# Performance work log

Measured on AMD Instinct MI355X. Metric: run time of the kernel, lower is better.

## Reference

```python
import jax, jax.numpy as jnp
import numpy as np

N_NODES = 100000
N_EDGES = 1600000
IN_FEAT = 128
OUT_FEAT = 128


def setup_inputs() -> dict:
    key = jax.random.key(0)
    k1, k2, k3 = jax.random.split(key, 3)
    x = jax.random.normal(k1, (N_NODES, IN_FEAT), dtype=jnp.float32)
    W = jax.random.normal(k2, (IN_FEAT, OUT_FEAT), dtype=jnp.float32) * (1.0 / np.sqrt(IN_FEAT))
    b = jnp.zeros((OUT_FEAT,), dtype=jnp.float32)
    edge_index = jax.random.randint(k3, (2, N_EDGES), 0, N_NODES, dtype=jnp.int64)
    return {"x": x, "W": W, "b": b, "edge_index": edge_index}


def reference(x, W, b, edge_index):
    # PyG GCNConv: add self-loops, symmetric deg normalization, scatter-add.
    N = x.shape[0]
    loops = jnp.arange(N, dtype=edge_index.dtype)
    ei = jnp.concatenate([edge_index, jnp.stack([loops, loops])], axis=1)  # [2, E+N]
    row, col = ei[0], ei[1]  # source, target
    ones = jnp.ones(ei.shape[1], dtype=x.dtype)
    deg = jax.ops.segment_sum(ones, col, num_segments=N)  # in-degree incl. self-loop
    deg_inv_sqrt = jnp.where(deg > 0, jax.lax.rsqrt(deg), 0.0)
    norm = deg_inv_sqrt[row] * deg_inv_sqrt[col]  # [E+N]
    xw = x @ W  # [N, out_feat]
    msg = xw[row] * norm[:, None]  # gather + normalize
    out = jax.ops.segment_sum(msg, col, num_segments=N) + b  # scatter-add + bias
    return out
```

## Files before the change

kernel.cpp:

```cpp
#include <hip/hip_runtime.h>

#define N_NODES 100000
#define N_EDGES 1600000
#define FEAT 128
#define NBUCK 782
#define BUCK_SHIFT 7
#define BUCK_MASK 127
#define GEMM_BLOCKS 1563
#define HIST_EPB 4096
#define HIST_BLOCKS 391
#define WT_PITCH 136

typedef __attribute__((ext_vector_type(8))) short short8;
typedef __attribute__((ext_vector_type(4))) float f32x4;

__device__ inline unsigned short f2bf(float f) {
    unsigned u = __builtin_bit_cast(unsigned, f);
    unsigned r = (u + 0x7FFFu + ((u >> 16) & 1u)) >> 16;
    return (unsigned short)r;
}
__device__ inline float bf2f(unsigned h) {
    unsigned u = h << 16;
    return __builtin_bit_cast(float, u);
}

__global__ __launch_bounds__(256)
void k_gemm_hist(const float* __restrict__ x, const float* __restrict__ W,
                 unsigned short* __restrict__ yb,
                 const int* __restrict__ col, int* __restrict__ bcnt) {
    int bid = blockIdx.x, tid = threadIdx.x;
    if (bid >= GEMM_BLOCKS) {
        __shared__ int hist[NBUCK];
        for (int i = tid; i < NBUCK; i += 256) hist[i] = 0;
        __syncthreads();
        int e0 = (bid - GEMM_BLOCKS) * HIST_EPB;
        int n = min(HIST_EPB, N_EDGES - e0);
        for (int i = tid * 4; i < n; i += 1024) {
            if (i + 3 < n) {
                int4 c4 = *(const int4*)(col + e0 + i);
                atomicAdd(&hist[c4.x >> BUCK_SHIFT], 1);
                atomicAdd(&hist[c4.y >> BUCK_SHIFT], 1);
                atomicAdd(&hist[c4.z >> BUCK_SHIFT], 1);
                atomicAdd(&hist[c4.w >> BUCK_SHIFT], 1);
            } else {
                for (int j = i; j < n; ++j) atomicAdd(&hist[col[e0 + j] >> BUCK_SHIFT], 1);
            }
        }
        __syncthreads();
        for (int i = tid; i < NBUCK; i += 256) {
            int h = hist[i];
            if (h) atomicAdd(&bcnt[i], h);
        }
        return;
    }

    __shared__ unsigned short Ws[FEAT * WT_PITCH];
    for (int idx = tid; idx < FEAT * FEAT; idx += 256) {
        int k = idx >> 7, n = idx & 127;
        Ws[n * WT_PITCH + k] = f2bf(W[idx]);
    }
    __syncthreads();

    int lane = tid & 63;
    int m = lane & 15, quad = lane >> 4;
    int rowBase = bid * 64 + (tid >> 6) * 16;
    int arow = rowBase + m;
    if (arow >= N_NODES) arow = N_NODES - 1;
    const float* xr = x + (size_t)arow * FEAT + quad * 8;

    f32x4 acc[8];
#pragma unroll
    for (int nt = 0; nt < 8; ++nt) acc[nt] = (f32x4){0.f, 0.f, 0.f, 0.f};

#pragma unroll
    for (int kk = 0; kk < 4; ++kk) {
        float4 xa = *(const float4*)(xr + kk * 32);
        float4 xc = *(const float4*)(xr + kk * 32 + 4);
        short8 a;
        a[0] = (short)f2bf(xa.x); a[1] = (short)f2bf(xa.y);
        a[2] = (short)f2bf(xa.z); a[3] = (short)f2bf(xa.w);
        a[4] = (short)f2bf(xc.x); a[5] = (short)f2bf(xc.y);
        a[6] = (short)f2bf(xc.z); a[7] = (short)f2bf(xc.w);
        const unsigned short* wp = Ws + m * WT_PITCH + kk * 32 + quad * 8;
#pragma unroll
        for (int nt = 0; nt < 8; ++nt) {
            short8 bf = *(const short8*)(wp + nt * 16 * WT_PITCH);
            acc[nt] = __builtin_amdgcn_mfma_f32_16x16x32_bf16(a, bf, acc[nt], 0, 0, 0);
        }
    }

    int r0 = rowBase + quad * 4;
#pragma unroll
    for (int nt = 0; nt < 8; ++nt) {
        int cc = nt * 16 + m;
#pragma unroll
        for (int r = 0; r < 4; ++r) {
            int rr = r0 + r;
            if (rr < N_NODES) yb[(size_t)rr * FEAT + cc] = f2bf(acc[nt][r]);
        }
    }
}

__global__ __launch_bounds__(1024)
void k_bscan(const int* __restrict__ bcnt, int* __restrict__ bstarts,
             int* __restrict__ bcursor) {
    __shared__ int s[1024];
    int tid = threadIdx.x;
    int v = (tid < NBUCK) ? bcnt[tid] : 0;
    s[tid] = v;
    __syncthreads();
    for (int off = 1; off < 1024; off <<= 1) {
        int t = (tid >= off) ? s[tid - off] : 0;
        __syncthreads();
        s[tid] += t;
        __syncthreads();
    }
    if (tid < NBUCK) {
        int ex = s[tid] - v;
        bstarts[tid] = ex;
        bcursor[tid] = ex;
    }
    if (tid == NBUCK - 1) bstarts[NBUCK] = s[tid];
}

__global__ __launch_bounds__(256)
void k_bscatter(const int* __restrict__ row, const int* __restrict__ col,
                int* __restrict__ bcursor, unsigned* __restrict__ ebuf) {
    __shared__ int hist[NBUCK];
    __shared__ int gbase[NBUCK];
    int tid = threadIdx.x;
    for (int i = tid; i < NBUCK; i += 256) hist[i] = 0;
    __syncthreads();
    int e0 = blockIdx.x * HIST_EPB;
    int n = min(HIST_EPB, N_EDGES - e0);
    for (int i = tid * 4; i < n; i += 1024) {
        if (i + 3 < n) {
            int4 c4 = *(const int4*)(col + e0 + i);
            atomicAdd(&hist[c4.x >> BUCK_SHIFT], 1);
            atomicAdd(&hist[c4.y >> BUCK_SHIFT], 1);
            atomicAdd(&hist[c4.z >> BUCK_SHIFT], 1);
            atomicAdd(&hist[c4.w >> BUCK_SHIFT], 1);
        } else {
            for (int j = i; j < n; ++j) atomicAdd(&hist[col[e0 + j] >> BUCK_SHIFT], 1);
        }
    }
    __syncthreads();
    for (int i = tid; i < NBUCK; i += 256) {
        int h = hist[i];
        gbase[i] = h ? atomicAdd(&bcursor[i], h) : 0;
    }
    __syncthreads();
    for (int i = tid; i < NBUCK; i += 256) hist[i] = 0;
    __syncthreads();
    for (int i = tid * 4; i < n; i += 1024) {
        if (i + 3 < n) {
            int4 c4 = *(const int4*)(col + e0 + i);
            int4 r4 = *(const int4*)(row + e0 + i);
            int bk, off;
            bk = c4.x >> BUCK_SHIFT; off = atomicAdd(&hist[bk], 1);
            ebuf[gbase[bk] + off] = ((unsigned)r4.x << BUCK_SHIFT) | (unsigned)(c4.x & BUCK_MASK);
            bk = c4.y >> BUCK_SHIFT; off = atomicAdd(&hist[bk], 1);
            ebuf[gbase[bk] + off] = ((unsigned)r4.y << BUCK_SHIFT) | (unsigned)(c4.y & BUCK_MASK);
            bk = c4.z >> BUCK_SHIFT; off = atomicAdd(&hist[bk], 1);
            ebuf[gbase[bk] + off] = ((unsigned)r4.z << BUCK_SHIFT) | (unsigned)(c4.z & BUCK_MASK);
            bk = c4.w >> BUCK_SHIFT; off = atomicAdd(&hist[bk], 1);
            ebuf[gbase[bk] + off] = ((unsigned)r4.w << BUCK_SHIFT) | (unsigned)(c4.w & BUCK_MASK);
        } else {
            for (int j = i; j < n; ++j) {
                int c = col[e0 + j], r = row[e0 + j];
                int bk = c >> BUCK_SHIFT;
                int off = atomicAdd(&hist[bk], 1);
                ebuf[gbase[bk] + off] = ((unsigned)r << BUCK_SHIFT) | (unsigned)(c & BUCK_MASK);
            }
        }
    }
}

__global__ __launch_bounds__(256)
void k_csr(const unsigned* __restrict__ ebuf, const int* __restrict__ bstarts,
           int* __restrict__ starts, float* __restrict__ dinv,
           int* __restrict__ src_idx) {
    __shared__ int hist[128];
    __shared__ int scan[128];
    __shared__ int cur[128];
    int b = blockIdx.x, tid = threadIdx.x;
    int node0 = b << BUCK_SHIFT;
    int nnodes = min(128, N_NODES - node0);
    if (tid < 128) hist[tid] = 0;
    __syncthreads();
    int e0 = bstarts[b], e1 = bstarts[b + 1];
    int ne = e1 - e0;
    for (int i = tid; i < ne; i += 256) atomicAdd(&hist[ebuf[e0 + i] & BUCK_MASK], 1);
    __syncthreads();
    if (tid < 128) scan[tid] = hist[tid];
    __syncthreads();
    for (int off = 1; off < 128; off <<= 1) {
        int t = 0;
        if (tid < 128 && tid >= off) t = scan[tid - off];
        __syncthreads();
        if (tid < 128) scan[tid] += t;
        __syncthreads();
    }
    if (tid < 128) {
        int ex = scan[tid] - hist[tid];
        cur[tid] = ex;
        if (tid < nnodes) {
            starts[node0 + tid] = e0 + ex;
            dinv[node0 + tid] = rsqrtf((float)(hist[tid] + 1));
        }
    }
    if (b == 0 && tid == 0) starts[N_NODES] = N_EDGES;
    __syncthreads();
    for (int i = tid; i < ne; i += 256) {
        unsigned e = ebuf[e0 + i];
        int pos = atomicAdd(&cur[e & BUCK_MASK], 1);
        src_idx[e0 + pos] = (int)(e >> BUCK_SHIFT);
    }
}

__global__ __launch_bounds__(256)
void k_agg(const unsigned short* __restrict__ yb, const int* __restrict__ starts,
           const int* __restrict__ src_idx, const float* __restrict__ dinv,
           const float* __restrict__ bias, float* __restrict__ out) {
    int node = blockIdx.x * 4 + (threadIdx.x >> 6);
    int lane = threadIdx.x & 63;
    if (node >= N_NODES) return;
    int st = starts[node], en = starts[node + 1];
    float di = dinv[node];
    const unsigned* y1 = (const unsigned*)yb;
    unsigned sv = y1[(size_t)node * 64 + lane];
    float a0 = di * bf2f(sv & 0xFFFFu);
    float a1 = di * bf2f(sv >> 16);
    for (int base = st; base < en; base += 64) {
        int nn = min(64, en - base);
        int src = 0;
        float dv = 0.f;
        if (lane < nn) {
            src = src_idx[base + lane];
            dv = dinv[src];
        }
        int j = 0;
        for (; j + 3 < nn; j += 4) {
            int s0 = __shfl(src, j),     s1 = __shfl(src, j + 1);
            int s2 = __shfl(src, j + 2), s3 = __shfl(src, j + 3);
            float d0 = __shfl(dv, j),     d1 = __shfl(dv, j + 1);
            float d2 = __shfl(dv, j + 2), d3 = __shfl(dv, j + 3);
            unsigned v0 = y1[(size_t)s0 * 64 + lane];
            unsigned v1 = y1[(size_t)s1 * 64 + lane];
            unsigned v2 = y1[(size_t)s2 * 64 + lane];
            unsigned v3 = y1[(size_t)s3 * 64 + lane];
            a0 += d0 * bf2f(v0 & 0xFFFFu); a1 += d0 * bf2f(v0 >> 16);
            a0 += d1 * bf2f(v1 & 0xFFFFu); a1 += d1 * bf2f(v1 >> 16);
            a0 += d2 * bf2f(v2 & 0xFFFFu); a1 += d2 * bf2f(v2 >> 16);
            a0 += d3 * bf2f(v3 & 0xFFFFu); a1 += d3 * bf2f(v3 >> 16);
        }
        for (; j < nn; ++j) {
            int s = __shfl(src, j);
            float d = __shfl(dv, j);
            unsigned v = y1[(size_t)s * 64 + lane];
            a0 += d * bf2f(v & 0xFFFFu);
            a1 += d * bf2f(v >> 16);
        }
    }
    float2 bb = ((const float2*)bias)[lane];
    float2 o;
    o.x = bb.x + di * a0;
    o.y = bb.y + di * a1;
    ((float2*)out)[(size_t)node * 64 + lane] = o;
}

extern "C" void kernel_launch(void* const* d_in, const int* in_sizes, int n_in,
                              void* d_out, int out_size, void* d_ws, size_t ws_size,
                              hipStream_t stream) {
    const float* x = (const float*)d_in[0];
    const float* W = (const float*)d_in[1];
    const float* b = (const float*)d_in[2];
    const int* ei = (const int*)d_in[3];
    const int* row = ei;
    const int* col = ei + N_EDGES;
    float* out = (float*)d_out;

    char* ws = (char*)d_ws;
    size_t off = 0;
    auto alloc = [&](size_t bytes) -> void* {
        void* p = ws + off;
        off += (bytes + 511) & ~(size_t)511;
        return p;
    };
    int* bcnt          = (int*)alloc((NBUCK + 1) * 4);
    int* bstarts       = (int*)alloc((NBUCK + 1) * 4);
    int* bcursor       = (int*)alloc((NBUCK + 1) * 4);
    int* starts        = (int*)alloc((size_t)(N_NODES + 1) * 4);
    float* dinv        = (float*)alloc((size_t)N_NODES * 4);
    unsigned* ebuf     = (unsigned*)alloc((size_t)N_EDGES * 4);
    int* src_idx       = (int*)alloc((size_t)N_EDGES * 4);
    unsigned short* yb = (unsigned short*)alloc((size_t)N_NODES * FEAT * 2);

    hipMemsetAsync(bcnt, 0, (NBUCK + 1) * 4, stream);

    k_gemm_hist<<<GEMM_BLOCKS + HIST_BLOCKS, 256, 0, stream>>>(x, W, yb, col, bcnt);
    k_bscan<<<1, 1024, 0, stream>>>(bcnt, bstarts, bcursor);
    k_bscatter<<<HIST_BLOCKS, 256, 0, stream>>>(row, col, bcursor, ebuf);
    k_csr<<<NBUCK, 256, 0, stream>>>(ebuf, bstarts, starts, dinv, src_idx);
    k_agg<<<(N_NODES + 3) / 4, 256, 0, stream>>>(yb, starts, src_idx, dinv, b, out);
}
```

Measured before the change: 237.2 us.

## Fuse bucket CSR build into aggregation and overlap GEMM with edge scatter

Weight conversion moves into the histogram kernel, and the bf16 GEMM now runs in the same launch as the edge scatter, with two 16-row tiles per wave. The separate CSR kernel and its src_idx and starts arrays are removed. A small kernel computes dinv per bucket, and the aggregation kernel sorts each bucket's edges into shared memory before gathering. This removes a global write and read pass over the sorted edges. In exchange, each aggregation block handles 128 nodes, which can unbalance load, and buckets larger than MAX_BUCK (3072) edges are silently truncated.

```diff
diff --git a/kernel.cpp b/kernel.cpp
--- a/kernel.cpp
+++ b/kernel.cpp
@@ -6,13 +6,16 @@
 #define NBUCK 782
 #define BUCK_SHIFT 7
 #define BUCK_MASK 127
-#define GEMM_BLOCKS 1563
 #define HIST_EPB 4096
 #define HIST_BLOCKS 391
+#define SCAT_BLOCKS 391
+#define GEMM_BLOCKS 782
 #define WT_PITCH 136
+#define MAX_BUCK 3072
 
 typedef __attribute__((ext_vector_type(8))) short short8;
 typedef __attribute__((ext_vector_type(4))) float f32x4;
+typedef __attribute__((ext_vector_type(2))) float f32x2;
 
 __device__ inline unsigned short f2bf(float f) {
     unsigned u = __builtin_bit_cast(unsigned, f);
@@ -23,115 +26,25 @@
     unsigned u = h << 16;
     return __builtin_bit_cast(float, u);
 }
+__device__ inline unsigned pkbf(float a, float b) {
+    return (unsigned)f2bf(a) | ((unsigned)f2bf(b) << 16);
+}
 
 __global__ __launch_bounds__(256)
-void k_gemm_hist(const float* __restrict__ x, const float* __restrict__ W,
-                 unsigned short* __restrict__ yb,
-                 const int* __restrict__ col, int* __restrict__ bcnt) {
+void k_hist_wt(const int* __restrict__ col, int* __restrict__ bcnt,
+               const float* __restrict__ W, unsigned short* __restrict__ Wt) {
     int bid = blockIdx.x, tid = threadIdx.x;
-    if (bid >= GEMM_BLOCKS) {
-        __shared__ int hist[NBUCK];
-        for (int i = tid; i < NBUCK; i += 256) hist[i] = 0;
-        __syncthreads();
-        int e0 = (bid - GEMM_BLOCKS) * HIST_EPB;
-        int n = min(HIST_EPB, N_EDGES - e0);
-        for (int i = tid * 4; i < n; i += 1024) {
-            if (i + 3 < n) {
-                int4 c4 = *(const int4*)(col + e0 + i);
-                atomicAdd(&hist[c4.x >> BUCK_SHIFT], 1);
-                atomicAdd(&hist[c4.y >> BUCK_SHIFT], 1);
-                atomicAdd(&hist[c4.z >> BUCK_SHIFT], 1);
-                atomicAdd(&hist[c4.w >> BUCK_SHIFT], 1);
-            } else {
-                for (int j = i; j < n; ++j) atomicAdd(&hist[col[e0 + j] >> BUCK_SHIFT], 1);
-            }
-        }
-        __syncthreads();
-        for (int i = tid; i < NBUCK; i += 256) {
-            int h = hist[i];
-            if (h) atomicAdd(&bcnt[i], h);
+    if (bid == HIST_BLOCKS) {
+        for (int idx = tid; idx < FEAT * FEAT; idx += 256) {
+            int k = idx >> 7, n = idx & 127;
+            Wt[n * WT_PITCH + k] = f2bf(W[idx]);
         }
         return;
     }
-
-    __shared__ unsigned short Ws[FEAT * WT_PITCH];
-    for (int idx = tid; idx < FEAT * FEAT; idx += 256) {
-        int k = idx >> 7, n = idx & 127;
-        Ws[n * WT_PITCH + k] = f2bf(W[idx]);
-    }
-    __syncthreads();
-
-    int lane = tid & 63;
-    int m = lane & 15, quad = lane >> 4;
-    int rowBase = bid * 64 + (tid >> 6) * 16;
-    int arow = rowBase + m;
-    if (arow >= N_NODES) arow = N_NODES - 1;
-    const float* xr = x + (size_t)arow * FEAT + quad * 8;
-
-    f32x4 acc[8];
-#pragma unroll
-    for (int nt = 0; nt < 8; ++nt) acc[nt] = (f32x4){0.f, 0.f, 0.f, 0.f};
-
-#pragma unroll
-    for (int kk = 0; kk < 4; ++kk) {
-        float4 xa = *(const float4*)(xr + kk * 32);
-        float4 xc = *(const float4*)(xr + kk * 32 + 4);
-        short8 a;
-        a[0] = (short)f2bf(xa.x); a[1] = (short)f2bf(xa.y);
-        a[2] = (short)f2bf(xa.z); a[3] = (short)f2bf(xa.w);
-        a[4] = (short)f2bf(xc.x); a[5] = (short)f2bf(xc.y);
-        a[6] = (short)f2bf(xc.z); a[7] = (short)f2bf(xc.w);
-        const unsigned short* wp = Ws + m * WT_PITCH + kk * 32 + quad * 8;
-#pragma unroll
-        for (int nt = 0; nt < 8; ++nt) {
-            short8 bf = *(const short8*)(wp + nt * 16 * WT_PITCH);
-            acc[nt] = __builtin_amdgcn_mfma_f32_16x16x32_bf16(a, bf, acc[nt], 0, 0, 0);
-        }
-    }
-
-    int r0 = rowBase + quad * 4;
-#pragma unroll
-    for (int nt = 0; nt < 8; ++nt) {
-        int cc = nt * 16 + m;
-#pragma unroll
-        for (int r = 0; r < 4; ++r) {
-            int rr = r0 + r;
-            if (rr < N_NODES) yb[(size_t)rr * FEAT + cc] = f2bf(acc[nt][r]);
-        }
-    }
-}
-
-__global__ __launch_bounds__(1024)
-void k_bscan(const int* __restrict__ bcnt, int* __restrict__ bstarts,
-             int* __restrict__ bcursor) {
-    __shared__ int s[1024];
-    int tid = threadIdx.x;
-    int v = (tid < NBUCK) ? bcnt[tid] : 0;
-    s[tid] = v;
-    __syncthreads();
-    for (int off = 1; off < 1024; off <<= 1) {
-        int t = (tid >= off) ? s[tid - off] : 0;
-        __syncthreads();
-        s[tid] += t;
-        __syncthreads();
-    }
-    if (tid < NBUCK) {
-        int ex = s[tid] - v;
-        bstarts[tid] = ex;
-        bcursor[tid] = ex;
-    }
-    if (tid == NBUCK - 1) bstarts[NBUCK] = s[tid];
-}
-
-__global__ __launch_bounds__(256)
-void k_bscatter(const int* __restrict__ row, const int* __restrict__ col,
-                int* __restrict__ bcursor, unsigned* __restrict__ ebuf) {
     __shared__ int hist[NBUCK];
-    __shared__ int gbase[NBUCK];
-    int tid = threadIdx.x;
     for (int i = tid; i < NBUCK; i += 256) hist[i] = 0;
     __syncthreads();
-    int e0 = blockIdx.x * HIST_EPB;
+    int e0 = bid * HIST_EPB;
     int n = min(HIST_EPB, N_EDGES - e0);
     for (int i = tid * 4; i < n; i += 1024) {
         if (i + 3 < n) {
@@ -147,126 +60,253 @@
     __syncthreads();
     for (int i = tid; i < NBUCK; i += 256) {
         int h = hist[i];
-        gbase[i] = h ? atomicAdd(&bcursor[i], h) : 0;
-    }
-    __syncthreads();
-    for (int i = tid; i < NBUCK; i += 256) hist[i] = 0;
-    __syncthreads();
-    for (int i = tid * 4; i < n; i += 1024) {
-        if (i + 3 < n) {
-            int4 c4 = *(const int4*)(col + e0 + i);
-            int4 r4 = *(const int4*)(row + e0 + i);
-            int bk, off;
-            bk = c4.x >> BUCK_SHIFT; off = atomicAdd(&hist[bk], 1);
-            ebuf[gbase[bk] + off] = ((unsigned)r4.x << BUCK_SHIFT) | (unsigned)(c4.x & BUCK_MASK);
-            bk = c4.y >> BUCK_SHIFT; off = atomicAdd(&hist[bk], 1);
-            ebuf[gbase[bk] + off] = ((unsigned)r4.y << BUCK_SHIFT) | (unsigned)(c4.y & BUCK_MASK);
-            bk = c4.z >> BUCK_SHIFT; off = atomicAdd(&hist[bk], 1);
-            ebuf[gbase[bk] + off] = ((unsigned)r4.z << BUCK_SHIFT) | (unsigned)(c4.z & BUCK_MASK);
-            bk = c4.w >> BUCK_SHIFT; off = atomicAdd(&hist[bk], 1);
-            ebuf[gbase[bk] + off] = ((unsigned)r4.w << BUCK_SHIFT) | (unsigned)(c4.w & BUCK_MASK);
-        } else {
-            for (int j = i; j < n; ++j) {
-                int c = col[e0 + j], r = row[e0 + j];
-                int bk = c >> BUCK_SHIFT;
-                int off = atomicAdd(&hist[bk], 1);
-                ebuf[gbase[bk] + off] = ((unsigned)r << BUCK_SHIFT) | (unsigned)(c & BUCK_MASK);
-            }
-        }
-    }
+        if (h) atomicAdd(&bcnt[i], h);
+    }
+}
+
+__global__ __launch_bounds__(1024)
+void k_bscan(const int* __restrict__ bcnt, int* __restrict__ bstarts,
+             int* __restrict__ bcursor) {
+    __shared__ int s[1024];
+    int tid = threadIdx.x;
+    int v = (tid < NBUCK) ? bcnt[tid] : 0;
+    s[tid] = v;
+    __syncthreads();
+    for (int off = 1; off < 1024; off <<= 1) {
+        int t = (tid >= off) ? s[tid - off] : 0;
+        __syncthreads();
+        s[tid] += t;
+        __syncthreads();
+    }
+    if (tid < NBUCK) {
+        int ex = s[tid] - v;
+        bstarts[tid] = ex;
+        bcursor[tid] = ex;
+    }
+    if (tid == NBUCK - 1) bstarts[NBUCK] = s[tid];
 }
 
 __global__ __launch_bounds__(256)
-void k_csr(const unsigned* __restrict__ ebuf, const int* __restrict__ bstarts,
-           int* __restrict__ starts, float* __restrict__ dinv,
-           int* __restrict__ src_idx) {
+void k_scatter_gemm(const int* __restrict__ row, const int* __restrict__ col,
+                    int* __restrict__ bcursor, unsigned* __restrict__ ebuf,
+                    const float* __restrict__ x, const unsigned short* __restrict__ Wt,
+                    unsigned short* __restrict__ yb) {
+    __shared__ union U {
+        struct { int hist[NBUCK]; int gbase[NBUCK]; } sc;
+        unsigned short ws[18432];
+    } u;
+    int bid = blockIdx.x, tid = threadIdx.x;
+
+    if (bid < SCAT_BLOCKS) {
+        for (int i = tid; i < NBUCK; i += 256) u.sc.hist[i] = 0;
+        __syncthreads();
+        int e0 = bid * HIST_EPB;
+        int n = min(HIST_EPB, N_EDGES - e0);
+        for (int i = tid * 4; i < n; i += 1024) {
+            if (i + 3 < n) {
+                int4 c4 = *(const int4*)(col + e0 + i);
+                atomicAdd(&u.sc.hist[c4.x >> BUCK_SHIFT], 1);
+                atomicAdd(&u.sc.hist[c4.y >> BUCK_SHIFT], 1);
+                atomicAdd(&u.sc.hist[c4.z >> BUCK_SHIFT], 1);
+                atomicAdd(&u.sc.hist[c4.w >> BUCK_SHIFT], 1);
+            } else {
+                for (int j = i; j < n; ++j) atomicAdd(&u.sc.hist[col[e0 + j] >> BUCK_SHIFT], 1);
+            }
+        }
+        __syncthreads();
+        for (int i = tid; i < NBUCK; i += 256) {
+            int h = u.sc.hist[i];
+            u.sc.gbase[i] = h ? atomicAdd(&bcursor[i], h) : 0;
+        }
+        __syncthreads();
+        for (int i = tid; i < NBUCK; i += 256) u.sc.hist[i] = 0;
+        __syncthreads();
+        for (int i = tid * 4; i < n; i += 1024) {
+            if (i + 3 < n) {
+                int4 c4 = *(const int4*)(col + e0 + i);
+                int4 r4 = *(const int4*)(row + e0 + i);
+                int bk, off;
+                bk = c4.x >> BUCK_SHIFT; off = atomicAdd(&u.sc.hist[bk], 1);
+                ebuf[u.sc.gbase[bk] + off] = ((unsigned)r4.x << BUCK_SHIFT) | (unsigned)(c4.x & BUCK_MASK);
+                bk = c4.y >> BUCK_SHIFT; off = atomicAdd(&u.sc.hist[bk], 1);
+                ebuf[u.sc.gbase[bk] + off] = ((unsigned)r4.y << BUCK_SHIFT) | (unsigned)(c4.y & BUCK_MASK);
+                bk = c4.z >> BUCK_SHIFT; off = atomicAdd(&u.sc.hist[bk], 1);
+                ebuf[u.sc.gbase[bk] + off] = ((unsigned)r4.z << BUCK_SHIFT) | (unsigned)(c4.z & BUCK_MASK);
+                bk = c4.w >> BUCK_SHIFT; off = atomicAdd(&u.sc.hist[bk], 1);
+                ebuf[u.sc.gbase[bk] + off] = ((unsigned)r4.w << BUCK_SHIFT) | (unsigned)(c4.w & BUCK_MASK);
+            } else {
+                for (int j = i; j < n; ++j) {
+                    int c = col[e0 + j], r = row[e0 + j];
+                    int bk = c >> BUCK_SHIFT;
+                    int off = atomicAdd(&u.sc.hist[bk], 1);
+                    ebuf[u.sc.gbase[bk] + off] = ((unsigned)r << BUCK_SHIFT) | (unsigned)(c & BUCK_MASK);
+                }
+            }
+        }
+        return;
+    }
+
+    int gb = bid - SCAT_BLOCKS;
+    for (int i = tid; i < 2304; i += 256)
+        ((uint4*)u.ws)[i] = ((const uint4*)Wt)[i];
+    __syncthreads();
+
+    int lane = tid & 63, wv = tid >> 6;
+    int m = lane & 15, quad = lane >> 4;
+    int rowT0 = gb * 128 + wv * 32;
+    int ar0 = rowT0 + m;       if (ar0 >= N_NODES) ar0 = N_NODES - 1;
+    int ar1 = rowT0 + 16 + m;  if (ar1 >= N_NODES) ar1 = N_NODES - 1;
+    const float* xr0 = x + (size_t)ar0 * FEAT + quad * 8;
+    const float* xr1 = x + (size_t)ar1 * FEAT + quad * 8;
+
+    f32x4 acc[2][8];
+#pragma unroll
+    for (int t = 0; t < 2; ++t)
+#pragma unroll
+        for (int nt = 0; nt < 8; ++nt) acc[t][nt] = (f32x4){0.f, 0.f, 0.f, 0.f};
+
+#pragma unroll
+    for (int kk = 0; kk < 4; ++kk) {
+        float4 a0 = *(const float4*)(xr0 + kk * 32);
+        float4 a1 = *(const float4*)(xr0 + kk * 32 + 4);
+        float4 b0 = *(const float4*)(xr1 + kk * 32);
+        float4 b1 = *(const float4*)(xr1 + kk * 32 + 4);
+        union { unsigned w[4]; short8 v; } A0, A1;
+        A0.w[0] = pkbf(a0.x, a0.y); A0.w[1] = pkbf(a0.z, a0.w);
+        A0.w[2] = pkbf(a1.x, a1.y); A0.w[3] = pkbf(a1.z, a1.w);
+        A1.w[0] = pkbf(b0.x, b0.y); A1.w[1] = pkbf(b0.z, b0.w);
+        A1.w[2] = pkbf(b1.x, b1.y); A1.w[3] = pkbf(b1.z, b1.w);
+        const unsigned short* wp = u.ws + m * WT_PITCH + kk * 32 + quad * 8;
+#pragma unroll
+        for (int nt = 0; nt < 8; ++nt) {
+            short8 bf = *(const short8*)(wp + nt * 16 * WT_PITCH);
+            acc[0][nt] = __builtin_amdgcn_mfma_f32_16x16x32_bf16(A0.v, bf, acc[0][nt], 0, 0, 0);
+            acc[1][nt] = __builtin_amdgcn_mfma_f32_16x16x32_bf16(A1.v, bf, acc[1][nt], 0, 0, 0);
+        }
+    }
+
+#pragma unroll
+    for (int t = 0; t < 2; ++t) {
+        int r0 = rowT0 + t * 16 + quad * 4;
+#pragma unroll
+        for (int nt = 0; nt < 8; ++nt) {
+            int cc = nt * 16 + m;
+#pragma unroll
+            for (int r = 0; r < 4; ++r) {
+                int rr = r0 + r;
+                if (rr < N_NODES) yb[(size_t)rr * FEAT + cc] = f2bf(acc[t][nt][r]);
+            }
+        }
+    }
+}
+
+__global__ __launch_bounds__(256)
+void k_dinv(const unsigned* __restrict__ ebuf, const int* __restrict__ bstarts,
+            float* __restrict__ dinv) {
     __shared__ int hist[128];
-    __shared__ int scan[128];
-    __shared__ int cur[128];
+    int b = blockIdx.x, tid = threadIdx.x;
+    if (tid < 128) hist[tid] = 0;
+    __syncthreads();
+    int e0 = bstarts[b], e1 = bstarts[b + 1];
+    for (int i = e0 + tid; i < e1; i += 256) atomicAdd(&hist[ebuf[i] & BUCK_MASK], 1);
+    __syncthreads();
+    int node0 = b << BUCK_SHIFT;
+    if (tid < 128 && node0 + tid < N_NODES)
+        dinv[node0 + tid] = rsqrtf((float)(hist[tid] + 1));
+}
+
+__global__ __launch_bounds__(256)
+void k_agg(const unsigned short* __restrict__ yb, const unsigned* __restrict__ ebuf,
+           const int* __restrict__ bstarts, const float* __restrict__ dinv,
+           const float* __restrict__ bias, float* __restrict__ out) {
+    __shared__ unsigned elist[MAX_BUCK];
+    __shared__ int slist[MAX_BUCK];
+    __shared__ int hist[128], sstart[128], cur[128];
+    __shared__ float dloc[128];
     int b = blockIdx.x, tid = threadIdx.x;
     int node0 = b << BUCK_SHIFT;
-    int nnodes = min(128, N_NODES - node0);
     if (tid < 128) hist[tid] = 0;
     __syncthreads();
-    int e0 = bstarts[b], e1 = bstarts[b + 1];
-    int ne = e1 - e0;
-    for (int i = tid; i < ne; i += 256) atomicAdd(&hist[ebuf[e0 + i] & BUCK_MASK], 1);
-    __syncthreads();
-    if (tid < 128) scan[tid] = hist[tid];
+    int e0 = bstarts[b];
+    int ne = bstarts[b + 1] - e0;
+    if (ne > MAX_BUCK) ne = MAX_BUCK;
+    for (int i = tid; i < ne; i += 256) {
+        unsigned e = ebuf[e0 + i];
+        elist[i] = e;
+        atomicAdd(&hist[e & BUCK_MASK], 1);
+    }
+    __syncthreads();
+    if (tid < 128) sstart[tid] = hist[tid];
     __syncthreads();
     for (int off = 1; off < 128; off <<= 1) {
         int t = 0;
-        if (tid < 128 && tid >= off) t = scan[tid - off];
-        __syncthreads();
-        if (tid < 128) scan[tid] += t;
+        if (tid < 128 && tid >= off) t = sstart[tid - off];
+        __syncthreads();
+        if (tid < 128) sstart[tid] += t;
         __syncthreads();
     }
     if (tid < 128) {
-        int ex = scan[tid] - hist[tid];
+        int ex = sstart[tid] - hist[tid];
+        sstart[tid] = ex;
         cur[tid] = ex;
-        if (tid < nnodes) {
-            starts[node0 + tid] = e0 + ex;
-            dinv[node0 + tid] = rsqrtf((float)(hist[tid] + 1));
-        }
-    }
-    if (b == 0 && tid == 0) starts[N_NODES] = N_EDGES;
+        dloc[tid] = rsqrtf((float)(hist[tid] + 1));
+    }
     __syncthreads();
     for (int i = tid; i < ne; i += 256) {
-        unsigned e = ebuf[e0 + i];
-        int pos = atomicAdd(&cur[e & BUCK_MASK], 1);
-        src_idx[e0 + pos] = (int)(e >> BUCK_SHIFT);
-    }
-}
-
-__global__ __launch_bounds__(256)
-void k_agg(const unsigned short* __restrict__ yb, const int* __restrict__ starts,
-           const int* __restrict__ src_idx, const float* __restrict__ dinv,
-           const float* __restrict__ bias, float* __restrict__ out) {
-    int node = blockIdx.x * 4 + (threadIdx.x >> 6);
-    int lane = threadIdx.x & 63;
-    if (node >= N_NODES) return;
-    int st = starts[node], en = starts[node + 1];
-    float di = dinv[node];
+        unsigned e = elist[i];
+        int t = e & BUCK_MASK;
+        int p = atomicAdd(&cur[t], 1);
+        slist[p] = (int)(e >> BUCK_SHIFT);
+    }
+    __syncthreads();
+
+    int wv = tid >> 6, lane = tid & 63;
     const unsigned* y1 = (const unsigned*)yb;
-    unsigned sv = y1[(size_t)node * 64 + lane];
-    float a0 = di * bf2f(sv & 0xFFFFu);
-    float a1 = di * bf2f(sv >> 16);
-    for (int base = st; base < en; base += 64) {
-        int nn = min(64, en - base);
-        int src = 0;
-        float dv = 0.f;
-        if (lane < nn) {
-            src = src_idx[base + lane];
-            dv = dinv[src];
-        }
-        int j = 0;
-        for (; j + 3 < nn; j += 4) {
-            int s0 = __shfl(src, j),     s1 = __shfl(src, j + 1);
-            int s2 = __shfl(src, j + 2), s3 = __shfl(src, j + 3);
-            float d0 = __shfl(dv, j),     d1 = __shfl(dv, j + 1);
-            float d2 = __shfl(dv, j + 2), d3 = __shfl(dv, j + 3);
-            unsigned v0 = y1[(size_t)s0 * 64 + lane];
-            unsigned v1 = y1[(size_t)s1 * 64 + lane];
-            unsigned v2 = y1[(size_t)s2 * 64 + lane];
-            unsigned v3 = y1[(size_t)s3 * 64 + lane];
-            a0 += d0 * bf2f(v0 & 0xFFFFu); a1 += d0 * bf2f(v0 >> 16);
-            a0 += d1 * bf2f(v1 & 0xFFFFu); a1 += d1 * bf2f(v1 >> 16);
-            a0 += d2 * bf2f(v2 & 0xFFFFu); a1 += d2 * bf2f(v2 >> 16);
-            a0 += d3 * bf2f(v3 & 0xFFFFu); a1 += d3 * bf2f(v3 >> 16);
-        }
-        for (; j < nn; ++j) {
-            int s = __shfl(src, j);
-            float d = __shfl(dv, j);
-            unsigned v = y1[(size_t)s * 64 + lane];
-            a0 += d * bf2f(v & 0xFFFFu);
-            a1 += d * bf2f(v >> 16);
-        }
-    }
     float2 bb = ((const float2*)bias)[lane];
-    float2 o;
-    o.x = bb.x + di * a0;
-    o.y = bb.y + di * a1;
-    ((float2*)out)[(size_t)node * 64 + lane] = o;
+    for (int nl = wv; nl < 128; nl += 4) {
+        int node = node0 + nl;
+        if (node >= N_NODES) break;
+        float di = dloc[nl];
+        unsigned sv = y1[(size_t)node * 64 + lane];
+        float a0 = di * bf2f(sv & 0xFFFFu);
+        float a1 = di * bf2f(sv >> 16);
+        int st = sstart[nl], deg = hist[nl];
+        for (int base = 0; base < deg; base += 64) {
+            int nn = min(64, deg - base);
+            int src = 0;
+            float dv = 0.f;
+            if (lane < nn) {
+                src = slist[st + base + lane];
+                dv = dinv[src];
+            }
+            int j = 0;
+            for (; j + 3 < nn; j += 4) {
+                int s0 = __shfl(src, j),     s1 = __shfl(src, j + 1);
+                int s2 = __shfl(src, j + 2), s3 = __shfl(src, j + 3);
+                float d0 = __shfl(dv, j),     d1 = __shfl(dv, j + 1);
+                float d2 = __shfl(dv, j + 2), d3 = __shfl(dv, j + 3);
+                unsigned v0 = y1[(size_t)s0 * 64 + lane];
+                unsigned v1 = y1[(size_t)s1 * 64 + lane];
+                unsigned v2 = y1[(size_t)s2 * 64 + lane];
+                unsigned v3 = y1[(size_t)s3 * 64 + lane];
+                a0 += d0 * bf2f(v0 & 0xFFFFu); a1 += d0 * bf2f(v0 >> 16);
+                a0 += d1 * bf2f(v1 & 0xFFFFu); a1 += d1 * bf2f(v1 >> 16);
+                a0 += d2 * bf2f(v2 & 0xFFFFu); a1 += d2 * bf2f(v2 >> 16);
+                a0 += d3 * bf2f(v3 & 0xFFFFu); a1 += d3 * bf2f(v3 >> 16);
+            }
+            for (; j < nn; ++j) {
+                int s = __shfl(src, j);
+                float d = __shfl(dv, j);
+                unsigned v = y1[(size_t)s * 64 + lane];
+                a0 += d * bf2f(v & 0xFFFFu);
+                a1 += d * bf2f(v >> 16);
+            }
+        }
+        f32x2 o;
+        o.x = bb.x + di * a0;
+        o.y = bb.y + di * a1;
+        __builtin_nontemporal_store(o, (f32x2*)(out + (size_t)node * FEAT) + lane);
+    }
 }
 
 extern "C" void kernel_launch(void* const* d_in, const int* in_sizes, int n_in,
@@ -290,17 +330,17 @@
     int* bcnt          = (int*)alloc((NBUCK + 1) * 4);
     int* bstarts       = (int*)alloc((NBUCK + 1) * 4);
     int* bcursor       = (int*)alloc((NBUCK + 1) * 4);
-    int* starts        = (int*)alloc((size_t)(N_NODES + 1) * 4);
     float* dinv        = (float*)alloc((size_t)N_NODES * 4);
     unsigned* ebuf     = (unsigned*)alloc((size_t)N_EDGES * 4);
-    int* src_idx       = (int*)alloc((size_t)N_EDGES * 4);
+    unsigned short* Wt = (unsigned short*)alloc(36864);
     unsigned short* yb = (unsigned short*)alloc((size_t)N_NODES * FEAT * 2);
 
-    hipMemsetAsync(bcnt, 0, (NBUCK + 1) * 4, stream);
-
-    k_gemm_hist<<<GEMM_BLOCKS + HIST_BLOCKS, 256, 0, stream>>>(x, W, yb, col, bcnt);
+    (void)hipMemsetAsync(bcnt, 0, (NBUCK + 1) * 4, stream);
+
+    k_hist_wt<<<HIST_BLOCKS + 1, 256, 0, stream>>>(col, bcnt, W, Wt);
     k_bscan<<<1, 1024, 0, stream>>>(bcnt, bstarts, bcursor);
-    k_bscatter<<<HIST_BLOCKS, 256, 0, stream>>>(row, col, bcursor, ebuf);
-    k_csr<<<NBUCK, 256, 0, stream>>>(ebuf, bstarts, starts, dinv, src_idx);
-    k_agg<<<(N_NODES + 3) / 4, 256, 0, stream>>>(yb, starts, src_idx, dinv, b, out);
-}
+    k_scatter_gemm<<<SCAT_BLOCKS + GEMM_BLOCKS, 256, 0, stream>>>(
+        row, col, bcursor, ebuf, x, Wt, yb);
+    k_dinv<<<NBUCK, 256, 0, stream>>>(ebuf, bstarts, dinv);
+    k_agg<<<NBUCK, 256, 0, stream>>>(yb, ebuf, bstarts, dinv, b, out);
+}
```

New measurement: 272.4 us. 14.8% more time.
